# Kernel tuning notes

Hardware: AMD Instinct MI355X
Metric: run time of the kernel (lower is better)

Reference implementation:

```python
import jax, jax.numpy as jnp
import numpy as np

# Dims matching init_kwargs: k=5, inplanes=512, planes=512, m=4, padding=None, stride=1
N, C, H, W = 32, 512, 56, 56
M = 4
CM = C // M          # 128, = group count (depthwise)
K1 = 5               # dynamic kernel size
K2 = 3               # atrous kernel size (dilation 2)
P2 = 512 // 2        # planes // 2


def setup_inputs() -> dict:
    key = jax.random.key(0)
    ks = jax.random.split(key, 13)
    s = lambda i, shape: jax.random.normal(ks[i], shape, jnp.float32) * 0.05
    return dict(
        x=jax.random.normal(ks[0], (N, C, H, W), jnp.float32),
        W_conv=s(1, (CM, C)), b_conv=s(2, (CM,)),        # self.conv (1x1)
        wk=s(3, (K1 * K1,)), bk=s(4, (K1 * K1,)),        # self.conv_kernel (1->k*k, 1x1)
        wck=s(5, ()), bck=s(6, ()),                      # self.conv_k (1->1, 1x1 scalar affine)
        wk2=s(7, (K2 * K2,)), bk2=s(8, (K2 * K2,)),      # self.conv_kernel2 (1->9)
        wck2=s(9, ()), bck2=s(10, ()),                   # self.conv_k2
        W_fuse=s(11, (P2, CM)), b_fuse=s(12, (P2,)),     # self.fuse (1x1)
    )


def _dw_conv(f, kern, dil, pad):
    # Per-sample depthwise conv: fold batch into groups -> single conv call.
    # f: [N, CM, H, W], kern: [N, CM, k, k]
    n, cm, h, w = f.shape
    fr = f.reshape(1, n * cm, h, w)
    kr = kern.reshape(n * cm, 1, kern.shape[-2], kern.shape[-1])
    o = jax.lax.conv_general_dilated(
        fr, kr, window_strides=(1, 1), padding=[(pad, pad), (pad, pad)],
        rhs_dilation=(dil, dil), feature_group_count=n * cm,
        dimension_numbers=('NCHW', 'OIHW', 'NCHW'))
    return o.reshape(n, cm, h, w)


def reference(x, W_conv, b_conv, wk, bk, wck, bck, wk2, bk2, wck2, bck2, W_fuse, b_fuse):
    # f = relu(conv(x));  g = relu(conv(avg_pool(x)))
    f = jax.nn.relu(jnp.einsum('nchw,oc->nohw', x, W_conv) + b_conv[None, :, None, None])
    g = jax.nn.relu(x.mean((2, 3)) @ W_conv.T + b_conv)  # [N, CM]
    # dynamic per-channel kernels: (g*wk + bk)*wck + bck, reshaped to [N, CM, k, k]
    kern1 = ((g[:, :, None] * wk + bk) * wck + bck).reshape(N, CM, K1, K1)
    kern2 = ((g[:, :, None] * wk2 + bk2) * wck2 + bck2).reshape(N, CM, K2, K2)
    o1 = _dw_conv(f, kern1, dil=1, pad=(K1 - 1) // 2)   # plain branch
    o2 = _dw_conv(f, kern2, dil=2, pad=2)               # atrous branch
    y1 = jnp.einsum('nchw,oc->nohw', o1, W_fuse) + b_fuse[None, :, None, None]
    y2 = jnp.einsum('nchw,oc->nohw', o2, W_fuse) + b_fuse[None, :, None, None]
    return jnp.concatenate([y1, y2], axis=1)  # [N, planes, H, W]
```

## Files before the change

### kernel.cpp

```cpp
#include <hip/hip_runtime.h>

typedef unsigned short u16;
typedef unsigned int   u32;

#define NB   32
#define CIN  512
#define CM   128
#define P2   256
#define HW   3136
#define HD   56

typedef __attribute__((ext_vector_type(8))) short           short8;
typedef __attribute__((ext_vector_type(8))) unsigned short  ushort8;
typedef __attribute__((ext_vector_type(4))) unsigned short  ushort4_t;
typedef __attribute__((ext_vector_type(4))) float           f32x4;

__device__ __forceinline__ float b2f(u16 u) {
    union { u32 i; float f; } v; v.i = ((u32)u) << 16; return v.f;
}
__device__ __forceinline__ u16 f2b(float f) {
    u32 u = __builtin_bit_cast(u32, f);
    u32 r = (u + 0x7fffu + ((u >> 16) & 1u)) >> 16;
    return (u16)r;
}

__global__ __launch_bounds__(256) void init_kernel(const float* __restrict__ Wc,
                                                   const float* __restrict__ Wf,
                                                   u16* __restrict__ Wcb,
                                                   u16* __restrict__ Wfb,
                                                   float* __restrict__ xm) {
    int i = blockIdx.x * 256 + threadIdx.x;
    if (i < CM * CIN) { Wcb[i] = f2b(Wc[i]); return; }
    i -= CM * CIN;
    if (i < P2 * CM) { Wfb[i] = f2b(Wf[i]); return; }
    i -= P2 * CM;
    if (i < NB * CIN) xm[i] = 0.f;
}

__global__ __launch_bounds__(128) void g_kernel(const float* __restrict__ Wc,
                                                const float* __restrict__ bc,
                                                const float* __restrict__ xm,
                                                float* __restrict__ g) {
    const int n = blockIdx.x, cm = threadIdx.x;
    __shared__ float xs[CIN];
    for (int i = threadIdx.x; i < CIN; i += 128)
        xs[i] = xm[n * CIN + i] * (1.0f / HW);
    __syncthreads();
    const float* wrow = Wc + (size_t)cm * CIN;
    float acc = 0.f;
    for (int c = 0; c < CIN; ++c) acc += wrow[c] * xs[c];
    acc += bc[cm];
    g[n * CM + cm] = fmaxf(acc, 0.f);
}

__global__ __launch_bounds__(256) void gemm1_kernel(
    const float* __restrict__ In,
    const u16* __restrict__ Wm, const float* __restrict__ bias,
    u16* __restrict__ Out, float* __restrict__ xm)
{
    __shared__ u16 ldsT[128 * 36];

    const int n    = blockIdx.z;
    const int hw0  = blockIdx.x * 128;
    const int mblk = blockIdx.y * 128;
    const int tid  = threadIdx.x;
    const int wave = tid >> 6, lane = tid & 63;
    const int wm   = (wave >> 1) * 64;
    const int wn   = (wave & 1) * 64;
    const int qa   = lane >> 4;
    const int l15  = lane & 15;

    f32x4 acc[4][4] = {};

    const int kpair = tid >> 4;
    const int c0    = (tid & 15) * 8;
    const int hwc   = hw0 + c0;
    const bool cok  = (hwc < HW);

    for (int k0 = 0; k0 < CIN; k0 += 32) {
        __syncthreads();
        u32 pk[8];
        {
            f32x4 a0 = {0,0,0,0}, a1 = {0,0,0,0}, d0 = {0,0,0,0}, d1 = {0,0,0,0};
            if (cok) {
                const float* p0 = In + (size_t)n * CIN * HW
                                + (size_t)(k0 + kpair * 2) * HW + hwc;
                a0 = *(const f32x4*)p0;
                a1 = *(const f32x4*)(p0 + 4);
                d0 = *(const f32x4*)(p0 + HW);
                d1 = *(const f32x4*)(p0 + HW + 4);
            }
            float fa[8] = {a0[0],a0[1],a0[2],a0[3],a1[0],a1[1],a1[2],a1[3]};
            float fb[8] = {d0[0],d0[1],d0[2],d0[3],d1[0],d1[1],d1[2],d1[3]};
            #pragma unroll
            for (int e = 0; e < 8; ++e) {
                u32 ua = __builtin_bit_cast(u32, fa[e]) + 0x8000u;
                u32 ub = __builtin_bit_cast(u32, fb[e]) + 0x8000u;
                pk[e] = __builtin_amdgcn_perm(ub, ua, 0x07060302u);
            }
            float s0 = fa[0]+fa[1]+fa[2]+fa[3]+fa[4]+fa[5]+fa[6]+fa[7];
            float s1 = fb[0]+fb[1]+fb[2]+fb[3]+fb[4]+fb[5]+fb[6]+fb[7];
            #pragma unroll
            for (int off = 8; off > 0; off >>= 1) {
                s0 += __shfl_xor(s0, off, 16);
                s1 += __shfl_xor(s1, off, 16);
            }
            if ((tid & 15) == 0) {
                atomicAdd(&xm[n * CIN + k0 + kpair * 2],     s0);
                atomicAdd(&xm[n * CIN + k0 + kpair * 2 + 1], s1);
            }
        }
        #pragma unroll
        for (int e = 0; e < 8; ++e)
            *(u32*)&ldsT[(c0 + e) * 36 + kpair * 2] = pk[e];
        __syncthreads();

        short8 a[4];
        #pragma unroll
        for (int mt = 0; mt < 4; ++mt) {
            int row = mblk + wm + mt * 16 + l15;
            a[mt] = *(const short8*)(Wm + (size_t)row * CIN + k0 + qa * 8);
        }
        #pragma unroll
        for (int nt = 0; nt < 4; ++nt) {
            int c = wn + nt * 16 + l15;
            union { ushort4_t h[2]; short8 v; } bu;
            bu.h[0] = *(const ushort4_t*)&ldsT[c * 36 + qa * 8];
            bu.h[1] = *(const ushort4_t*)&ldsT[c * 36 + qa * 8 + 4];
            short8 b = bu.v;
            #pragma unroll
            for (int mt = 0; mt < 4; ++mt)
                acc[mt][nt] = __builtin_amdgcn_mfma_f32_16x16x32_bf16(a[mt], b, acc[mt][nt], 0, 0, 0);
        }
    }

    const int r4 = qa * 4;
    #pragma unroll
    for (int nt = 0; nt < 4; ++nt) {
        int colhw = hw0 + wn + nt * 16 + l15;
        if (colhw >= HW) continue;
        #pragma unroll
        for (int mt = 0; mt < 4; ++mt) {
            int mbase = mblk + wm + mt * 16 + r4;
            #pragma unroll
            for (int r = 0; r < 4; ++r) {
                int m = mbase + r;
                float v = fmaxf(acc[mt][nt][r] + bias[m], 0.f);
                Out[((size_t)n * CM + m) * HW + colhw] = f2b(v);
            }
        }
    }
}

#define PD 60
__global__ __launch_bounds__(256) void dw_kernel(
    const u16* __restrict__ f, const float* __restrict__ g,
    const float* __restrict__ wk,  const float* __restrict__ bk,
    const float* __restrict__ wck, const float* __restrict__ bck,
    const float* __restrict__ wk2, const float* __restrict__ bk2,
    const float* __restrict__ wck2,const float* __restrict__ bck2,
    u16* __restrict__ o1, u16* __restrict__ o2)
{
    const int ncm = blockIdx.x;
    __shared__ float fpl[PD * PD];
    __shared__ float kc1[25], kc2[9];

    {
        f32x4 z = {0.f, 0.f, 0.f, 0.f};
        f32x4* fv = (f32x4*)fpl;
        for (int i = threadIdx.x; i < PD * PD / 4; i += 256) fv[i] = z;
    }
    const float gv = g[ncm];
    if (threadIdx.x < 25) {
        int t = threadIdx.x;
        kc1[t] = (gv * wk[t] + bk[t]) * wck[0] + bck[0];
    } else if (threadIdx.x >= 32 && threadIdx.x < 41) {
        int t = threadIdx.x - 32;
        kc2[t] = (gv * wk2[t] + bk2[t]) * wck2[0] + bck2[0];
    }
    __syncthreads();

    const size_t base = (size_t)ncm * HW;
    const u32* fp = (const u32*)(f + base);
    for (int i = threadIdx.x; i < HW / 2; i += 256) {
        u32 v = fp[i];
        int px = 2 * i;
        int h = px / HD, w = px - h * HD;
        float* dst = &fpl[(h + 2) * PD + (w + 2)];
        dst[0] = b2f((u16)v);
        dst[1] = b2f((u16)(v >> 16));
    }
    __syncthreads();

    u32* o1p = (u32*)(o1 + base);
    u32* o2p = (u32*)(o2 + base);
    for (int u = threadIdx.x; u < 392; u += 256) {
        int h  = u / 7;
        int gq = u - h * 7;
        int w0 = gq * 8;
        float a1[8] = {}, a2[8] = {};
        #pragma unroll
        for (int di = 0; di < 5; ++di) {
            const float* row = &fpl[(h + di) * PD + w0];
            float r[12];
            #pragma unroll
            for (int x = 0; x < 12; ++x) r[x] = row[x];
            #pragma unroll
            for (int j = 0; j < 5; ++j) {
                float kv = kc1[di * 5 + j];
                #pragma unroll
                for (int e = 0; e < 8; ++e) a1[e] = fmaf(kv, r[j + e], a1[e]);
            }
            if ((di & 1) == 0) {
                int i2 = di >> 1;
                #pragma unroll
                for (int j = 0; j < 3; ++j) {
                    float kv = kc2[i2 * 3 + j];
                    #pragma unroll
                    for (int e = 0; e < 8; ++e) a2[e] = fmaf(kv, r[2 * j + e], a2[e]);
                }
            }
        }
        int ob = (h * HD + w0) >> 1;
        #pragma unroll
        for (int e = 0; e < 4; ++e) {
            o1p[ob + e] = (u32)f2b(a1[2 * e]) | ((u32)f2b(a1[2 * e + 1]) << 16);
            o2p[ob + e] = (u32)f2b(a2[2 * e]) | ((u32)f2b(a2[2 * e + 1]) << 16);
        }
    }
}

#define FSTR 140
__global__ __launch_bounds__(256) void fuse_kernel(
    const u16* __restrict__ o1, const u16* __restrict__ o2,
    const u16* __restrict__ Wfb, const float* __restrict__ bias,
    float* __restrict__ out)
{
    __shared__ u16 ldsT[64 * FSTR];

    const int n   = blockIdx.z;
    const int br  = blockIdx.y;
    const u16* In = br ? o2 : o1;
    const int ch_off = br ? P2 : 0;
    const int hw0 = blockIdx.x * 64;
    const int tid = threadIdx.x;
    const int wave = tid >> 6, lane = tid & 63;
    const int wm  = wave * 64;
    const int qa  = lane >> 4, l15 = lane & 15;

    {
        const int c0 = (tid & 7) * 8;
        const int kp = tid >> 3;
        #pragma unroll
        for (int kk = 0; kk < CM; kk += 64) {
            const u16* p0 = In + (size_t)n * CM * HW + (size_t)(kk + 2 * kp) * HW + hw0 + c0;
            ushort8 v0 = *(const ushort8*)p0;
            ushort8 v1 = *(const ushort8*)(p0 + HW);
            #pragma unroll
            for (int e = 0; e < 8; ++e)
                *(u32*)&ldsT[(c0 + e) * FSTR + kk + 2 * kp] = (u32)v0[e] | ((u32)v1[e] << 16);
        }
    }
    __syncthreads();

    f32x4 acc[4][4] = {};
    #pragma unroll
    for (int q = 0; q < 4; ++q) {
        short8 a[4];
        #pragma unroll
        for (int mt = 0; mt < 4; ++mt) {
            int row = wm + mt * 16 + l15;
            a[mt] = *(const short8*)(Wfb + (size_t)row * CM + q * 32 + qa * 8);
        }
        #pragma unroll
        for (int nt = 0; nt < 4; ++nt) {
            int c = nt * 16 + l15;
            union { ushort4_t h[2]; short8 v; } bu;
            bu.h[0] = *(const ushort4_t*)&ldsT[c * FSTR + q * 32 + qa * 8];
            bu.h[1] = *(const ushort4_t*)&ldsT[c * FSTR + q * 32 + qa * 8 + 4];
            #pragma unroll
            for (int mt = 0; mt < 4; ++mt)
                acc[mt][nt] = __builtin_amdgcn_mfma_f32_16x16x32_bf16(a[mt], bu.v, acc[mt][nt], 0, 0, 0);
        }
    }

    const int r4 = qa * 4;
    #pragma unroll
    for (int nt = 0; nt < 4; ++nt) {
        int colhw = hw0 + nt * 16 + l15;
        #pragma unroll
        for (int mt = 0; mt < 4; ++mt) {
            int mbase = wm + mt * 16 + r4;
            #pragma unroll
            for (int r = 0; r < 4; ++r) {
                int m = mbase + r;
                float v = acc[mt][nt][r] + bias[m];
                out[((size_t)n * 512 + ch_off + m) * HW + colhw] = v;
            }
        }
    }
}

extern "C" void kernel_launch(void* const* d_in, const int* in_sizes, int n_in,
                              void* d_out, int out_size, void* d_ws, size_t ws_size,
                              hipStream_t stream) {
    const float* x     = (const float*)d_in[0];
    const float* Wconv = (const float*)d_in[1];
    const float* bconv = (const float*)d_in[2];
    const float* wk    = (const float*)d_in[3];
    const float* bk    = (const float*)d_in[4];
    const float* wck   = (const float*)d_in[5];
    const float* bck   = (const float*)d_in[6];
    const float* wk2   = (const float*)d_in[7];
    const float* bk2   = (const float*)d_in[8];
    const float* wck2  = (const float*)d_in[9];
    const float* bck2  = (const float*)d_in[10];
    const float* Wfuse = (const float*)d_in[11];
    const float* bfuse = (const float*)d_in[12];
    float* out = (float*)d_out;

    float* xm  = (float*)d_ws;
    float* g   = xm + NB * CIN;
    u16*   Wcb = (u16*)(g + NB * CM);
    u16*   Wfb = Wcb + CM * CIN;
    u16*   f   = Wfb + P2 * CM;
    u16*   o1  = f  + (size_t)NB * CM * HW;
    u16*   o2  = o1 + (size_t)NB * CM * HW;

    {
        int tot = CM * CIN + P2 * CM + NB * CIN;
        init_kernel<<<dim3((tot + 255) / 256), 256, 0, stream>>>(Wconv, Wfuse, Wcb, Wfb, xm);
    }
    gemm1_kernel<<<dim3(25, 1, NB), 256, 0, stream>>>(x, Wcb, bconv, f, xm);
    g_kernel<<<dim3(NB), 128, 0, stream>>>(Wconv, bconv, xm, g);
    dw_kernel<<<dim3(NB * CM), 256, 0, stream>>>(f, g, wk, bk, wck, bck,
                                                 wk2, bk2, wck2, bck2, o1, o2);
    fuse_kernel<<<dim3(49, 2, NB), 256, 0, stream>>>(o1, o2, Wfb, bfuse, out);
}
```

Before: 456.4 us.

## Fold pooled-branch into GEMM epilogue, swap MFMA operands for vector stores

The separate g_kernel and the per-K-step atomic sums of x are removed. Instead, the first GEMM epilogue reduces its pre-bias 1x1-conv outputs per output channel into a small buffer, and dw_kernel rebuilds g as relu(sum/HW + bias). This relies on the mean commuting with the linear conv, but it now uses bf16-rounded x and weights for g. Both GEMMs swap the MFMA A/B roles so each lane holds consecutive spatial outputs, which allows packed or vector stores. dw_kernel now zeroes only the padding border and loads 4 bf16 values per thread.

```diff
diff --git a/kernel.cpp b/kernel.cpp
--- a/kernel.cpp
+++ b/kernel.cpp
@@ -14,6 +14,7 @@
 typedef __attribute__((ext_vector_type(8))) unsigned short  ushort8;
 typedef __attribute__((ext_vector_type(4))) unsigned short  ushort4_t;
 typedef __attribute__((ext_vector_type(4))) float           f32x4;
+typedef __attribute__((ext_vector_type(2))) unsigned int    u32x2;
 
 __device__ __forceinline__ float b2f(u16 u) {
     union { u32 i; float f; } v; v.i = ((u32)u) << 16; return v.f;
@@ -28,41 +29,24 @@
                                                    const float* __restrict__ Wf,
                                                    u16* __restrict__ Wcb,
                                                    u16* __restrict__ Wfb,
-                                                   float* __restrict__ xm) {
+                                                   float* __restrict__ ym) {
     int i = blockIdx.x * 256 + threadIdx.x;
     if (i < CM * CIN) { Wcb[i] = f2b(Wc[i]); return; }
     i -= CM * CIN;
     if (i < P2 * CM) { Wfb[i] = f2b(Wf[i]); return; }
     i -= P2 * CM;
-    if (i < NB * CIN) xm[i] = 0.f;
-}
-
-__global__ __launch_bounds__(128) void g_kernel(const float* __restrict__ Wc,
-                                                const float* __restrict__ bc,
-                                                const float* __restrict__ xm,
-                                                float* __restrict__ g) {
-    const int n = blockIdx.x, cm = threadIdx.x;
-    __shared__ float xs[CIN];
-    for (int i = threadIdx.x; i < CIN; i += 128)
-        xs[i] = xm[n * CIN + i] * (1.0f / HW);
-    __syncthreads();
-    const float* wrow = Wc + (size_t)cm * CIN;
-    float acc = 0.f;
-    for (int c = 0; c < CIN; ++c) acc += wrow[c] * xs[c];
-    acc += bc[cm];
-    g[n * CM + cm] = fmaxf(acc, 0.f);
+    if (i < NB * CM) ym[i] = 0.f;
 }
 
 __global__ __launch_bounds__(256) void gemm1_kernel(
     const float* __restrict__ In,
     const u16* __restrict__ Wm, const float* __restrict__ bias,
-    u16* __restrict__ Out, float* __restrict__ xm)
+    u16* __restrict__ Out, float* __restrict__ ym)
 {
-    __shared__ u16 ldsT[128 * 36];
+    __shared__ u16 ldsT[128 * 40];
 
     const int n    = blockIdx.z;
     const int hw0  = blockIdx.x * 128;
-    const int mblk = blockIdx.y * 128;
     const int tid  = threadIdx.x;
     const int wave = tid >> 6, lane = tid & 63;
     const int wm   = (wave >> 1) * 64;
@@ -98,63 +82,58 @@
                 u32 ub = __builtin_bit_cast(u32, fb[e]) + 0x8000u;
                 pk[e] = __builtin_amdgcn_perm(ub, ua, 0x07060302u);
             }
-            float s0 = fa[0]+fa[1]+fa[2]+fa[3]+fa[4]+fa[5]+fa[6]+fa[7];
-            float s1 = fb[0]+fb[1]+fb[2]+fb[3]+fb[4]+fb[5]+fb[6]+fb[7];
-            #pragma unroll
-            for (int off = 8; off > 0; off >>= 1) {
-                s0 += __shfl_xor(s0, off, 16);
-                s1 += __shfl_xor(s1, off, 16);
-            }
-            if ((tid & 15) == 0) {
-                atomicAdd(&xm[n * CIN + k0 + kpair * 2],     s0);
-                atomicAdd(&xm[n * CIN + k0 + kpair * 2 + 1], s1);
-            }
         }
         #pragma unroll
         for (int e = 0; e < 8; ++e)
-            *(u32*)&ldsT[(c0 + e) * 36 + kpair * 2] = pk[e];
+            *(u32*)&ldsT[(c0 + e) * 40 + kpair * 2] = pk[e];
         __syncthreads();
 
-        short8 a[4];
-        #pragma unroll
-        for (int mt = 0; mt < 4; ++mt) {
-            int row = mblk + wm + mt * 16 + l15;
-            a[mt] = *(const short8*)(Wm + (size_t)row * CIN + k0 + qa * 8);
-        }
+        short8 b[4];
         #pragma unroll
         for (int nt = 0; nt < 4; ++nt) {
-            int c = wn + nt * 16 + l15;
-            union { ushort4_t h[2]; short8 v; } bu;
-            bu.h[0] = *(const ushort4_t*)&ldsT[c * 36 + qa * 8];
-            bu.h[1] = *(const ushort4_t*)&ldsT[c * 36 + qa * 8 + 4];
-            short8 b = bu.v;
-            #pragma unroll
-            for (int mt = 0; mt < 4; ++mt)
-                acc[mt][nt] = __builtin_amdgcn_mfma_f32_16x16x32_bf16(a[mt], b, acc[mt][nt], 0, 0, 0);
-        }
-    }
-
-    const int r4 = qa * 4;
+            int row = wm + nt * 16 + l15;
+            b[nt] = *(const short8*)(Wm + (size_t)row * CIN + k0 + qa * 8);
+        }
+        #pragma unroll
+        for (int ht = 0; ht < 4; ++ht) {
+            short8 a = *(const short8*)&ldsT[(wn + ht * 16 + l15) * 40 + qa * 8];
+            #pragma unroll
+            for (int nt = 0; nt < 4; ++nt)
+                acc[ht][nt] = __builtin_amdgcn_mfma_f32_16x16x32_bf16(a, b[nt], acc[ht][nt], 0, 0, 0);
+        }
+    }
+
     #pragma unroll
     for (int nt = 0; nt < 4; ++nt) {
-        int colhw = hw0 + wn + nt * 16 + l15;
-        if (colhw >= HW) continue;
-        #pragma unroll
-        for (int mt = 0; mt < 4; ++mt) {
-            int mbase = mblk + wm + mt * 16 + r4;
-            #pragma unroll
-            for (int r = 0; r < 4; ++r) {
-                int m = mbase + r;
-                float v = fmaxf(acc[mt][nt][r] + bias[m], 0.f);
-                Out[((size_t)n * CM + m) * HW + colhw] = f2b(v);
-            }
-        }
+        const int m = wm + nt * 16 + l15;
+        const float bv = bias[m];
+        float s = 0.f;
+        #pragma unroll
+        for (int ht = 0; ht < 4; ++ht) {
+            f32x4 v = acc[ht][nt];
+            s += v[0] + v[1] + v[2] + v[3];
+            int hwb = hw0 + wn + ht * 16;
+            if (hwb < HW) {
+                float v0 = fmaxf(v[0] + bv, 0.f);
+                float v1 = fmaxf(v[1] + bv, 0.f);
+                float v2 = fmaxf(v[2] + bv, 0.f);
+                float v3 = fmaxf(v[3] + bv, 0.f);
+                u32x2 pkv;
+                pkv.x = (u32)f2b(v0) | ((u32)f2b(v1) << 16);
+                pkv.y = (u32)f2b(v2) | ((u32)f2b(v3) << 16);
+                *(u32x2*)(Out + ((size_t)n * CM + m) * HW + hwb + qa * 4) = pkv;
+            }
+        }
+        s += __shfl_xor(s, 16);
+        s += __shfl_xor(s, 32);
+        if (lane < 16) atomicAdd(&ym[n * CM + m], s);
     }
 }
 
 #define PD 60
 __global__ __launch_bounds__(256) void dw_kernel(
-    const u16* __restrict__ f, const float* __restrict__ g,
+    const u16* __restrict__ f, const float* __restrict__ ym,
+    const float* __restrict__ bc,
     const float* __restrict__ wk,  const float* __restrict__ bk,
     const float* __restrict__ wck, const float* __restrict__ bck,
     const float* __restrict__ wk2, const float* __restrict__ bk2,
@@ -166,11 +145,16 @@
     __shared__ float kc1[25], kc2[9];
 
     {
-        f32x4 z = {0.f, 0.f, 0.f, 0.f};
-        f32x4* fv = (f32x4*)fpl;
-        for (int i = threadIdx.x; i < PD * PD / 4; i += 256) fv[i] = z;
-    }
-    const float gv = g[ncm];
+        int t = threadIdx.x;
+        if (t < 120) { fpl[t] = 0.f; fpl[58 * PD + t] = 0.f; }
+        else if (t < 232) {
+            int u = t - 120;
+            int r = 2 + (u >> 1), c = u & 1;
+            fpl[r * PD + c]      = 0.f;
+            fpl[r * PD + 58 + c] = 0.f;
+        }
+    }
+    const float gv = fmaxf(ym[ncm] * (1.0f / HW) + bc[ncm & (CM - 1)], 0.f);
     if (threadIdx.x < 25) {
         int t = threadIdx.x;
         kc1[t] = (gv * wk[t] + bk[t]) * wck[0] + bck[0];
@@ -181,14 +165,16 @@
     __syncthreads();
 
     const size_t base = (size_t)ncm * HW;
-    const u32* fp = (const u32*)(f + base);
-    for (int i = threadIdx.x; i < HW / 2; i += 256) {
-        u32 v = fp[i];
-        int px = 2 * i;
+    const u32x2* fp = (const u32x2*)(f + base);
+    for (int i = threadIdx.x; i < HW / 4; i += 256) {
+        u32x2 v = fp[i];
+        int px = 4 * i;
         int h = px / HD, w = px - h * HD;
         float* dst = &fpl[(h + 2) * PD + (w + 2)];
-        dst[0] = b2f((u16)v);
-        dst[1] = b2f((u16)(v >> 16));
+        dst[0] = b2f((u16)v.x);
+        dst[1] = b2f((u16)(v.x >> 16));
+        dst[2] = b2f((u16)v.y);
+        dst[3] = b2f((u16)(v.y >> 16));
     }
     __syncthreads();
 
@@ -266,37 +252,37 @@
     f32x4 acc[4][4] = {};
     #pragma unroll
     for (int q = 0; q < 4; ++q) {
-        short8 a[4];
-        #pragma unroll
-        for (int mt = 0; mt < 4; ++mt) {
-            int row = wm + mt * 16 + l15;
-            a[mt] = *(const short8*)(Wfb + (size_t)row * CM + q * 32 + qa * 8);
-        }
+        short8 b[4];
         #pragma unroll
         for (int nt = 0; nt < 4; ++nt) {
-            int c = nt * 16 + l15;
-            union { ushort4_t h[2]; short8 v; } bu;
-            bu.h[0] = *(const ushort4_t*)&ldsT[c * FSTR + q * 32 + qa * 8];
-            bu.h[1] = *(const ushort4_t*)&ldsT[c * FSTR + q * 32 + qa * 8 + 4];
-            #pragma unroll
-            for (int mt = 0; mt < 4; ++mt)
-                acc[mt][nt] = __builtin_amdgcn_mfma_f32_16x16x32_bf16(a[mt], bu.v, acc[mt][nt], 0, 0, 0);
-        }
-    }
-
-    const int r4 = qa * 4;
+            int row = wm + nt * 16 + l15;
+            b[nt] = *(const short8*)(Wfb + (size_t)row * CM + q * 32 + qa * 8);
+        }
+        #pragma unroll
+        for (int ht = 0; ht < 4; ++ht) {
+            int c = ht * 16 + l15;
+            union { ushort4_t h[2]; short8 v; } au;
+            au.h[0] = *(const ushort4_t*)&ldsT[c * FSTR + q * 32 + qa * 8];
+            au.h[1] = *(const ushort4_t*)&ldsT[c * FSTR + q * 32 + qa * 8 + 4];
+            #pragma unroll
+            for (int nt = 0; nt < 4; ++nt)
+                acc[ht][nt] = __builtin_amdgcn_mfma_f32_16x16x32_bf16(au.v, b[nt], acc[ht][nt], 0, 0, 0);
+        }
+    }
+
     #pragma unroll
     for (int nt = 0; nt < 4; ++nt) {
-        int colhw = hw0 + nt * 16 + l15;
-        #pragma unroll
-        for (int mt = 0; mt < 4; ++mt) {
-            int mbase = wm + mt * 16 + r4;
-            #pragma unroll
-            for (int r = 0; r < 4; ++r) {
-                int m = mbase + r;
-                float v = acc[mt][nt][r] + bias[m];
-                out[((size_t)n * 512 + ch_off + m) * HW + colhw] = v;
-            }
+        const int m = wm + nt * 16 + l15;
+        const float bv = bias[m];
+        float* orow = out + ((size_t)n * 512 + ch_off + m) * HW + hw0 + qa * 4;
+        #pragma unroll
+        for (int ht = 0; ht < 4; ++ht) {
+            f32x4 v;
+            v[0] = acc[ht][nt][0] + bv;
+            v[1] = acc[ht][nt][1] + bv;
+            v[2] = acc[ht][nt][2] + bv;
+            v[3] = acc[ht][nt][3] + bv;
+            *(f32x4*)(orow + ht * 16) = v;
         }
     }
 }
@@ -319,21 +305,19 @@
     const float* bfuse = (const float*)d_in[12];
     float* out = (float*)d_out;
 
-    float* xm  = (float*)d_ws;
-    float* g   = xm + NB * CIN;
-    u16*   Wcb = (u16*)(g + NB * CM);
+    float* ym  = (float*)d_ws;
+    u16*   Wcb = (u16*)(ym + NB * CM);
     u16*   Wfb = Wcb + CM * CIN;
     u16*   f   = Wfb + P2 * CM;
     u16*   o1  = f  + (size_t)NB * CM * HW;
     u16*   o2  = o1 + (size_t)NB * CM * HW;
 
     {
-        int tot = CM * CIN + P2 * CM + NB * CIN;
-        init_kernel<<<dim3((tot + 255) / 256), 256, 0, stream>>>(Wconv, Wfuse, Wcb, Wfb, xm);
-    }
-    gemm1_kernel<<<dim3(25, 1, NB), 256, 0, stream>>>(x, Wcb, bconv, f, xm);
-    g_kernel<<<dim3(NB), 128, 0, stream>>>(Wconv, bconv, xm, g);
-    dw_kernel<<<dim3(NB * CM), 256, 0, stream>>>(f, g, wk, bk, wck, bck,
+        int tot = CM * CIN + P2 * CM + NB * CM;
+        init_kernel<<<dim3((tot + 255) / 256), 256, 0, stream>>>(Wconv, Wfuse, Wcb, Wfb, ym);
+    }
+    gemm1_kernel<<<dim3(25, 1, NB), 256, 0, stream>>>(x, Wcb, bconv, f, ym);
+    dw_kernel<<<dim3(NB * CM), 256, 0, stream>>>(f, ym, bconv, wk, bk, wck, bck,
                                                  wk2, bk2, wck2, bck2, o1, o2);
     fuse_kernel<<<dim3(49, 2, NB), 256, 0, stream>>>(o1, o2, Wfb, bfuse, out);
 }
```

Measured after the change: 457.8 us. Within noise of the previous version (+0.3%).
